# Kernel tuning notes

Measured on AMD Instinct MI355X. Metric: run time of the kernel, lower is better.

The kernel has to match this reference:

```python
import jax, jax.numpy as jnp
import numpy as np

N = 1_048_576   # flattened tokens
C = 128         # classes
IGNORE = 0
GAMMA = 1.0     # FocalLoss bug: alpha default (1) becomes self.gamma
BETA = 1.0      # ClassficationAndMDCA: self.beta = alpha = 1.0


def setup_inputs() -> dict:
    key = jax.random.key(0)
    k1, k2 = jax.random.split(key)
    inputs = jax.random.normal(k1, (N, C), dtype=jnp.float32)
    targets = jax.random.randint(k2, (N,), 0, C, dtype=jnp.int64)
    return {"inputs": inputs, "targets": targets}


def reference(inputs, targets):
    # ignore_index filtering expressed as masked reductions (jit-friendly)
    mask = (targets != IGNORE)
    maskf = mask.astype(inputs.dtype)               # [N]
    nvalid = jnp.sum(maskf)

    # Focal loss: -(1-pt)^gamma * log pt, mean over valid tokens
    logp = jax.nn.log_softmax(inputs, axis=1)       # [N, C]
    logpt = jnp.take_along_axis(logp, targets[:, None], axis=1)[:, 0]  # [N]
    pt = jnp.exp(logpt)
    focal = -((1.0 - pt) ** GAMMA) * logpt
    loss_cls = jnp.sum(focal * maskf) / nvalid

    # MDCA: per-class |mean confidence - mean label frequency|, mean over classes
    probs = jnp.exp(logp)                           # softmax, reuse log_softmax
    avg_conf = jnp.sum(probs * maskf[:, None], axis=0) / nvalid        # [C]
    avg_count = jnp.zeros((C,), inputs.dtype).at[targets].add(maskf) / nvalid  # [C]
    loss_cal = jnp.mean(jnp.abs(avg_conf - avg_count))

    return loss_cls + BETA * loss_cal
```

## Files before the change

### kernel.cpp

```cpp
#include <hip/hip_runtime.h>

#define NC 128
#define BLOCK 256
#define GRID 1024
#define DEPTH 4
#define QBYTES 2048
#define WPB (BLOCK / 64)

typedef float f32x4 __attribute__((ext_vector_type(4)));

__global__ void cmdca_init(float* __restrict__ acc) {
    if (threadIdx.x < 260) acc[threadIdx.x] = 0.0f;
}

template <int CTRL>
__device__ __forceinline__ float dpp_add(float v) {
    int s = __builtin_amdgcn_update_dpp(0, __float_as_int(v), CTRL, 0xF, 0xF, true);
    return v + __int_as_float(s);
}
__device__ __forceinline__ float rowsum16(float v) {
    v = dpp_add<0x121>(v);
    v = dpp_add<0x122>(v);
    v = dpp_add<0x124>(v);
    v = dpp_add<0x128>(v);
    return v;
}

__global__ __launch_bounds__(BLOCK) void cmdca_main(const float* __restrict__ in,
                                                    const int* __restrict__ tgt,
                                                    float* __restrict__ acc,
                                                    int nrows) {
    const int lane = threadIdx.x & 63;
    const int l15  = lane & 15;
    const int sub  = lane >> 4;
    const int wid  = threadIdx.x >> 6;
    const int wave = blockIdx.x * WPB + wid;
    const int nwaves = GRID * WPB;
    const int qtot = nrows >> 2;

    __shared__ char  stage[WPB * DEPTH * QBYTES];
    __shared__ int   tstage[WPB * DEPTH * 64];
    __shared__ float sconf[NC];
    __shared__ float scnt[NC];
    __shared__ float sfn[2];

    char* wstage = stage  + wid * DEPTH * QBYTES;
    int*  wts    = tstage + wid * DEPTH * 64;

    for (int i = threadIdx.x; i < NC; i += BLOCK) { sconf[i] = 0.f; scnt[i] = 0.f; }
    if (threadIdx.x < 2) sfn[threadIdx.x] = 0.f;
    __syncthreads();

    float conf[8] = {0.f, 0.f, 0.f, 0.f, 0.f, 0.f, 0.f, 0.f};
    float focal = 0.f, nval = 0.f;

    const int n = (qtot > wave) ? (qtot - 1 - wave) / nwaves + 1 : 0;

    auto stg = [&](int j, int slot) {
        size_t q = (size_t)wave + (size_t)j * nwaves;
        const char* g = (const char*)in + q * QBYTES + lane * 16;
        __builtin_amdgcn_global_load_lds(
            (const __attribute__((address_space(1))) void*)g,
            (__attribute__((address_space(3))) void*)(wstage + slot * QBYTES),
            16, 0, 0);
        __builtin_amdgcn_global_load_lds(
            (const __attribute__((address_space(1))) void*)(g + 1024),
            (__attribute__((address_space(3))) void*)(wstage + slot * QBYTES + 1024),
            16, 0, 0);
        __builtin_amdgcn_global_load_lds(
            (const __attribute__((address_space(1))) void*)(tgt + 4 * q + (lane & 3)),
            (__attribute__((address_space(3))) void*)(wts + slot * 64),
            4, 0, 0);
    };

    auto cmp = [&](int slot) {
        const char* b = wstage + slot * QBYTES + sub * 512 + l15 * 32;
        f32x4 xa = *(const f32x4*)b;
        f32x4 xb = *(const f32x4*)(b + 16);
        int t = wts[slot * 64 + sub];
        const int te = t & 7;
        float s01 = (te & 1) ? xa.y : xa.x;
        float s23 = (te & 1) ? xa.w : xa.z;
        float s45 = (te & 1) ? xb.y : xb.x;
        float s67 = (te & 1) ? xb.w : xb.z;
        float s03 = (te & 2) ? s23 : s01;
        float s47 = (te & 2) ? s67 : s45;
        float xsel = (te & 4) ? s47 : s03;
        float e0 = __expf(xa.x), e1 = __expf(xa.y), e2 = __expf(xa.z), e3 = __expf(xa.w);
        float e4 = __expf(xb.x), e5 = __expf(xb.y), e6 = __expf(xb.z), e7 = __expf(xb.w);
        float s8 = ((e0 + e1) + (e2 + e3)) + ((e4 + e5) + (e6 + e7));
        float s = rowsum16(s8);
        float invs = __builtin_amdgcn_rcpf(s);
        float logZ = __logf(s);
        int srcl = (lane & 48) | (t >> 3);
        float xt = __int_as_float(
            __builtin_amdgcn_ds_bpermute(srcl << 2, __float_as_int(xsel)));
        float logpt = xt - logZ;
        float pt = __expf(logpt);
        float valid = (t != 0) ? 1.0f : 0.0f;
        float vs = valid * invs;
        conf[0] += vs * e0; conf[1] += vs * e1; conf[2] += vs * e2; conf[3] += vs * e3;
        conf[4] += vs * e4; conf[5] += vs * e5; conf[6] += vs * e6; conf[7] += vs * e7;
        if (l15 == 0) {
            nval  += valid;
            focal += valid * (pt - 1.0f) * logpt;
            if (valid != 0.0f) atomicAdd(&scnt[t], 1.0f);
        }
    };

    for (int jp = 0; jp < n && jp < DEPTH - 1; ++jp) stg(jp, jp);
    int j = 0;
    for (; j + (DEPTH - 1) < n; ++j) {
        stg(j + DEPTH - 1, (j + DEPTH - 1) & (DEPTH - 1));
        asm volatile("s_waitcnt vmcnt(9)" ::: "memory");
        cmp(j & (DEPTH - 1));
    }
    for (; j < n; ++j) {
        int after = n - 1 - j;
        if (after >= 2)      { asm volatile("s_waitcnt vmcnt(6)" ::: "memory"); }
        else if (after == 1) { asm volatile("s_waitcnt vmcnt(3)" ::: "memory"); }
        else                 { asm volatile("s_waitcnt vmcnt(0)" ::: "memory"); }
        cmp(j & (DEPTH - 1));
    }

    __syncthreads();
    const int cb = 8 * l15;
    atomicAdd(&sconf[cb + 0], conf[0]);
    atomicAdd(&sconf[cb + 1], conf[1]);
    atomicAdd(&sconf[cb + 2], conf[2]);
    atomicAdd(&sconf[cb + 3], conf[3]);
    atomicAdd(&sconf[cb + 4], conf[4]);
    atomicAdd(&sconf[cb + 5], conf[5]);
    atomicAdd(&sconf[cb + 6], conf[6]);
    atomicAdd(&sconf[cb + 7], conf[7]);
    if (l15 == 0) {
        atomicAdd(&sfn[0], focal);
        atomicAdd(&sfn[1], nval);
    }
    __syncthreads();
    if (threadIdx.x < NC) {
        atomicAdd(&acc[threadIdx.x],      sconf[threadIdx.x]);
        atomicAdd(&acc[NC + threadIdx.x], scnt[threadIdx.x]);
    }
    if (threadIdx.x == 0) {
        atomicAdd(&acc[2 * NC],     sfn[0]);
        atomicAdd(&acc[2 * NC + 1], sfn[1]);
    }
}

__global__ void cmdca_fin(const float* __restrict__ acc, float* __restrict__ out) {
    int c = threadIdx.x;
    float nvalid = acc[2 * NC + 1];
    float diff = fabsf(acc[c] - acc[NC + c]) / nvalid;
    #pragma unroll
    for (int o = 32; o; o >>= 1) diff += __shfl_xor(diff, o);
    __shared__ float sh[2];
    if ((threadIdx.x & 63) == 0) sh[threadIdx.x >> 6] = diff;
    __syncthreads();
    if (threadIdx.x == 0) {
        float loss_cal = (sh[0] + sh[1]) / (float)NC;
        float loss_cls = acc[2 * NC] / nvalid;
        out[0] = loss_cls + loss_cal;
    }
}

extern "C" void kernel_launch(void* const* d_in, const int* in_sizes, int n_in,
                              void* d_out, int out_size, void* d_ws, size_t ws_size,
                              hipStream_t stream) {
    const float* in  = (const float*)d_in[0];
    const int*   tgt = (const int*)d_in[1];
    float* out = (float*)d_out;
    float* acc = (float*)d_ws;
    int nrows = in_sizes[0] / NC;

    hipLaunchKernelGGL(cmdca_init, dim3(1), dim3(512), 0, stream, acc);
    hipLaunchKernelGGL(cmdca_main, dim3(GRID), dim3(BLOCK), 0, stream, in, tgt, acc, nrows);
    hipLaunchKernelGGL(cmdca_fin,  dim3(1), dim3(NC), 0, stream, acc, out);
}
```

Baseline: 117.7 us.

## Process two rows per wave with 32 lanes each and preload targets once

```diff
diff --git a/kernel.cpp b/kernel.cpp
--- a/kernel.cpp
+++ b/kernel.cpp
@@ -2,9 +2,9 @@
 
 #define NC 128
 #define BLOCK 256
-#define GRID 1024
+#define GRID 2048
 #define DEPTH 4
-#define QBYTES 2048
+#define GBYTES 1024
 #define WPB (BLOCK / 64)
 
 typedef float f32x4 __attribute__((ext_vector_type(4)));
@@ -31,68 +31,61 @@
                                                     float* __restrict__ acc,
                                                     int nrows) {
     const int lane = threadIdx.x & 63;
-    const int l15  = lane & 15;
-    const int sub  = lane >> 4;
+    const int l31  = lane & 31;
+    const int half = lane >> 5;
     const int wid  = threadIdx.x >> 6;
     const int wave = blockIdx.x * WPB + wid;
     const int nwaves = GRID * WPB;
-    const int qtot = nrows >> 2;
+    const int ptot = nrows >> 1;
 
-    __shared__ char  stage[WPB * DEPTH * QBYTES];
-    __shared__ int   tstage[WPB * DEPTH * 64];
+    __shared__ char  stage[WPB * DEPTH * GBYTES];
+    __shared__ int   tall[WPB * 64 * 2];
     __shared__ float sconf[NC];
     __shared__ float scnt[NC];
     __shared__ float sfn[2];
 
-    char* wstage = stage  + wid * DEPTH * QBYTES;
-    int*  wts    = tstage + wid * DEPTH * 64;
+    char* wstage = stage + wid * DEPTH * GBYTES;
+    int*  wtall  = tall  + wid * 128;
 
     for (int i = threadIdx.x; i < NC; i += BLOCK) { sconf[i] = 0.f; scnt[i] = 0.f; }
     if (threadIdx.x < 2) sfn[threadIdx.x] = 0.f;
     __syncthreads();
 
-    float conf[8] = {0.f, 0.f, 0.f, 0.f, 0.f, 0.f, 0.f, 0.f};
+    float conf[4] = {0.f, 0.f, 0.f, 0.f};
     float focal = 0.f, nval = 0.f;
 
-    const int n = (qtot > wave) ? (qtot - 1 - wave) / nwaves + 1 : 0;
+    const int n = (ptot > wave) ? (ptot - 1 - wave) / nwaves + 1 : 0;
+
+    {
+        size_t p = (size_t)wave + (size_t)lane * nwaves;
+        if (p >= (size_t)ptot) p = (size_t)ptot - 1;
+        int2 tv = *reinterpret_cast<const int2*>(tgt + 2 * p);
+        *reinterpret_cast<int2*>(&wtall[2 * lane]) = tv;
+    }
 
     auto stg = [&](int j, int slot) {
-        size_t q = (size_t)wave + (size_t)j * nwaves;
-        const char* g = (const char*)in + q * QBYTES + lane * 16;
+        size_t p = (size_t)wave + (size_t)j * nwaves;
+        const char* g = (const char*)in + p * GBYTES + lane * 16;
         __builtin_amdgcn_global_load_lds(
             (const __attribute__((address_space(1))) void*)g,
-            (__attribute__((address_space(3))) void*)(wstage + slot * QBYTES),
+            (__attribute__((address_space(3))) void*)(wstage + slot * GBYTES),
             16, 0, 0);
-        __builtin_amdgcn_global_load_lds(
-            (const __attribute__((address_space(1))) void*)(g + 1024),
-            (__attribute__((address_space(3))) void*)(wstage + slot * QBYTES + 1024),
-            16, 0, 0);
-        __builtin_amdgcn_global_load_lds(
-            (const __attribute__((address_space(1))) void*)(tgt + 4 * q + (lane & 3)),
-            (__attribute__((address_space(3))) void*)(wts + slot * 64),
-            4, 0, 0);
     };
 
-    auto cmp = [&](int slot) {
-        const char* b = wstage + slot * QBYTES + sub * 512 + l15 * 32;
-        f32x4 xa = *(const f32x4*)b;
-        f32x4 xb = *(const f32x4*)(b + 16);
-        int t = wts[slot * 64 + sub];
-        const int te = t & 7;
-        float s01 = (te & 1) ? xa.y : xa.x;
-        float s23 = (te & 1) ? xa.w : xa.z;
-        float s45 = (te & 1) ? xb.y : xb.x;
-        float s67 = (te & 1) ? xb.w : xb.z;
-        float s03 = (te & 2) ? s23 : s01;
-        float s47 = (te & 2) ? s67 : s45;
-        float xsel = (te & 4) ? s47 : s03;
-        float e0 = __expf(xa.x), e1 = __expf(xa.y), e2 = __expf(xa.z), e3 = __expf(xa.w);
-        float e4 = __expf(xb.x), e5 = __expf(xb.y), e6 = __expf(xb.z), e7 = __expf(xb.w);
-        float s8 = ((e0 + e1) + (e2 + e3)) + ((e4 + e5) + (e6 + e7));
-        float s = rowsum16(s8);
+    auto cmp = [&](int slot, int j) {
+        const f32x4 x = *(const f32x4*)(wstage + slot * GBYTES + lane * 16);
+        int t = wtall[2 * j + half];
+        const int te = t & 3;
+        float s01 = (te & 1) ? x.y : x.x;
+        float s23 = (te & 1) ? x.w : x.z;
+        float xsel = (te & 2) ? s23 : s01;
+        float e0 = __expf(x.x), e1 = __expf(x.y), e2 = __expf(x.z), e3 = __expf(x.w);
+        float s16 = rowsum16((e0 + e1) + (e2 + e3));
+        float s = s16 + __int_as_float(
+            __builtin_amdgcn_ds_swizzle(__float_as_int(s16), 0x401F));
         float invs = __builtin_amdgcn_rcpf(s);
         float logZ = __logf(s);
-        int srcl = (lane & 48) | (t >> 3);
+        int srcl = (lane & 32) + (t >> 2);
         float xt = __int_as_float(
             __builtin_amdgcn_ds_bpermute(srcl << 2, __float_as_int(xsel)));
         float logpt = xt - logZ;
@@ -100,40 +93,35 @@
         float valid = (t != 0) ? 1.0f : 0.0f;
         float vs = valid * invs;
         conf[0] += vs * e0; conf[1] += vs * e1; conf[2] += vs * e2; conf[3] += vs * e3;
-        conf[4] += vs * e4; conf[5] += vs * e5; conf[6] += vs * e6; conf[7] += vs * e7;
-        if (l15 == 0) {
+        if (l31 == 0) {
             nval  += valid;
             focal += valid * (pt - 1.0f) * logpt;
-            if (valid != 0.0f) atomicAdd(&scnt[t], 1.0f);
         }
+        if (valid != 0.0f && l31 == (t >> 2)) atomicAdd(&scnt[t], 1.0f);
     };
 
     for (int jp = 0; jp < n && jp < DEPTH - 1; ++jp) stg(jp, jp);
     int j = 0;
     for (; j + (DEPTH - 1) < n; ++j) {
         stg(j + DEPTH - 1, (j + DEPTH - 1) & (DEPTH - 1));
-        asm volatile("s_waitcnt vmcnt(9)" ::: "memory");
-        cmp(j & (DEPTH - 1));
+        asm volatile("s_waitcnt vmcnt(3)" ::: "memory");
+        cmp(j & (DEPTH - 1), j);
     }
     for (; j < n; ++j) {
         int after = n - 1 - j;
-        if (after >= 2)      { asm volatile("s_waitcnt vmcnt(6)" ::: "memory"); }
-        else if (after == 1) { asm volatile("s_waitcnt vmcnt(3)" ::: "memory"); }
+        if (after >= 2)      { asm volatile("s_waitcnt vmcnt(2)" ::: "memory"); }
+        else if (after == 1) { asm volatile("s_waitcnt vmcnt(1)" ::: "memory"); }
         else                 { asm volatile("s_waitcnt vmcnt(0)" ::: "memory"); }
-        cmp(j & (DEPTH - 1));
+        cmp(j & (DEPTH - 1), j);
     }
 
     __syncthreads();
-    const int cb = 8 * l15;
+    const int cb = 4 * l31;
     atomicAdd(&sconf[cb + 0], conf[0]);
     atomicAdd(&sconf[cb + 1], conf[1]);
     atomicAdd(&sconf[cb + 2], conf[2]);
     atomicAdd(&sconf[cb + 3], conf[3]);
-    atomicAdd(&sconf[cb + 4], conf[4]);
-    atomicAdd(&sconf[cb + 5], conf[5]);
-    atomicAdd(&sconf[cb + 6], conf[6]);
-    atomicAdd(&sconf[cb + 7], conf[7]);
-    if (l15 == 0) {
+    if (l31 == 0) {
         atomicAdd(&sfn[0], focal);
         atomicAdd(&sfn[1], nval);
     }
```

Result: slower. 143.9 us (+22.2%).
